# Kernel tuning notes

Measured on AMD Instinct MI355X. Metric: run time of the kernel, lower is better.

Reference implementation:

```python
import jax, jax.numpy as jnp
import numpy as np

N = 20000
E = 160000
H = 4      # heads
C = 128    # per-head out channels (hidden_dim)
HID = 128


def setup_inputs() -> dict:
    key = jax.random.key(0)
    ks = jax.random.split(key, 24)
    inp = {}
    inp["x"] = jax.random.normal(ks[0], (8,), jnp.float32)
    inp["des"] = jax.random.normal(ks[1], (N, 768), jnp.float32)
    inp["tweet"] = jax.random.normal(ks[2], (N, 768), jnp.float32)
    inp["num_prop"] = jax.random.normal(ks[3], (N, 5), jnp.float32)
    inp["cat_prop"] = jax.random.normal(ks[4], (N, 1), jnp.float32)
    inp["edge_index"] = jax.random.randint(ks[5], (2, E), 0, N, dtype=jnp.int64)
    inp["target_node_idx"] = 123
    s = lambda fan_in: 1.0 / np.sqrt(fan_in)
    u = lambda k, shp, b: jax.random.uniform(k, shp, jnp.float32, -b, b)
    inp["W_des"] = u(ks[6], (768, 32), s(768)); inp["b_des"] = u(ks[7], (32,), s(768))
    inp["W_tw"] = u(ks[8], (768, 32), s(768)); inp["b_tw"] = u(ks[9], (32,), s(768))
    inp["W_np"] = u(ks[10], (5, 32), s(5));   inp["b_np"] = u(ks[11], (32,), s(5))
    inp["W_cp"] = u(ks[12], (1, 32), s(1));   inp["b_cp"] = u(ks[13], (32,), s(1))
    inp["W_gat"] = u(ks[14], (HID, H * C), s(HID))      # GATConv lin (no bias)
    inp["att_src"] = u(ks[15], (H, C), s(C))
    inp["att_dst"] = u(ks[16], (H, C), s(C))
    inp["b_gat"] = jnp.zeros((C,), jnp.float32)
    inp["W_o1"] = u(ks[17], (HID + 8, 64), s(HID + 8)); inp["b_o1"] = u(ks[18], (64,), s(HID + 8))
    inp["W_o2"] = u(ks[19], (64, 5), s(64));            inp["b_o2"] = u(ks[20], (5,), s(64))
    return inp


def _gat_conv(feature, edge_index, W_gat, att_src, att_dst, b_gat):
    # add self-loops (PyG default)
    loops = jnp.arange(N, dtype=edge_index.dtype)
    src = jnp.concatenate([edge_index[0], loops])
    dst = jnp.concatenate([edge_index[1], loops])
    h = (feature @ W_gat).reshape(N, H, C)                 # [N,H,C]
    a_src = jnp.einsum("nhc,hc->nh", h, att_src)           # [N,H]
    a_dst = jnp.einsum("nhc,hc->nh", h, att_dst)
    e = jax.nn.leaky_relu(a_src[src] + a_dst[dst], 0.2)    # [E+N,H]
    m = jax.ops.segment_max(e, dst, num_segments=N)        # segment softmax (stable)
    ex = jnp.exp(e - m[dst])
    denom = jax.ops.segment_sum(ex, dst, num_segments=N)
    alpha = ex / denom[dst]                                # [E+N,H]
    out = jax.ops.segment_sum(alpha[:, :, None] * h[src], dst, num_segments=N)  # [N,H,C]
    return out.mean(axis=1) + b_gat                        # concat=False -> mean heads


def reference(x, des, tweet, num_prop, cat_prop, edge_index, target_node_idx,
              W_des, b_des, W_tw, b_tw, W_np, b_np, W_cp, b_cp,
              W_gat, att_src, att_dst, b_gat, W_o1, b_o1, W_o2, b_o2):
    lrelu = jax.nn.leaky_relu  # slope 0.01 (nn.LeakyReLU default)
    d = lrelu(des @ W_des + b_des)
    t = lrelu(tweet @ W_tw + b_tw)
    n = lrelu(num_prop @ W_np + b_np)
    c = lrelu(cat_prop @ W_cp + b_cp)
    feature = jnp.concatenate([d, t, n, c], axis=1)        # [N,128]
    gat_out = _gat_conv(feature, edge_index, W_gat, att_src, att_dst, b_gat)
    target_feat = gat_out[target_node_idx]                 # [128]
    combined = jnp.concatenate([target_feat, x], axis=0)   # [136]
    hmid = jax.nn.relu(combined @ W_o1 + b_o1)
    return hmid @ W_o2 + b_o2                              # [5]
```

## Files before the change

### kernel.cpp

```cpp
#include <hip/hip_runtime.h>
#include <math.h>

#define HEADS 4
#define CDIM 128
#define HDIM 512
#define FEAT 128
#define NBS 128
#define NT 512
#define REG 8
#define TGT_SID (NBS * REG)
#define NMAX 64

__global__ __launch_bounds__(NT)
void scan_process_kernel(const float* __restrict__ des, const float* __restrict__ tw,
                         const float* __restrict__ npr, const float* __restrict__ cpr,
                         const float* __restrict__ Wd, const float* __restrict__ bd,
                         const float* __restrict__ Wt, const float* __restrict__ bt,
                         const float* __restrict__ Wn, const float* __restrict__ bn,
                         const float* __restrict__ Wc, const float* __restrict__ bc,
                         const float* __restrict__ Wg, const float* __restrict__ Wo1,
                         const float* __restrict__ att_src, const float* __restrict__ att_dst,
                         const int* __restrict__ ei, int E,
                         const int* __restrict__ tgt_p,
                         int* __restrict__ blockCounts,
                         float* __restrict__ aS, float* __restrict__ aD,
                         float* __restrict__ h_all) {
    __shared__ float sdes[768];
    __shared__ float stw[768];
    __shared__ float snp8[8];
    __shared__ float sfeat[FEAT];
    __shared__ float part[NT];
    __shared__ float pr[2 * HDIM];
    __shared__ int   lmatch[REG];
    __shared__ int   lcount;

    const int tid = threadIdx.x;
    const int b = blockIdx.x;
    const int tgt = *tgt_p;
    const int wv = tid >> 6, lane = tid & 63;

    auto process_node = [&](int node, int sid, bool isTgt) {
        if (tid < 192) {
            ((float4*)sdes)[tid] = ((const float4*)(des + (size_t)node * 768))[tid];
            ((float4*)stw)[tid]  = ((const float4*)(tw  + (size_t)node * 768))[tid];
        } else if (tid < 197) {
            snp8[tid - 192] = npr[node * 5 + (tid - 192)];
        } else if (tid == 197) {
            snp8[5] = cpr[node];
        }
        __syncthreads();

        {
            const int half = tid >> 8;
            const int t2 = tid & 255;
            const int j = t2 & 31, ch = t2 >> 5;
            const float* W = half ? Wt : Wd;
            const float* S = half ? stw : sdes;
            const float* wp = W + (size_t)(ch * 96) * 32 + j;
            const float* sp = S + ch * 96;
            float p = 0.f;
            #pragma unroll 16
            for (int k = 0; k < 96; ++k) p = fmaf(sp[k], wp[(size_t)k * 32], p);
            part[tid] = p;
        }
        __syncthreads();
        if (tid < 32) {
            float a = bd[tid];
            #pragma unroll
            for (int c2 = 0; c2 < 8; ++c2) a += part[c2 * 32 + tid];
            sfeat[tid] = a > 0.f ? a : 0.01f * a;
        } else if (tid < 64) {
            const int jj = tid - 32;
            float a = bt[jj];
            #pragma unroll
            for (int c2 = 0; c2 < 8; ++c2) a += part[256 + c2 * 32 + jj];
            sfeat[32 + jj] = a > 0.f ? a : 0.01f * a;
        } else if (tid < 96) {
            const int jj = tid - 64;
            float a = bn[jj];
            #pragma unroll
            for (int k = 0; k < 5; ++k) a = fmaf(snp8[k], Wn[k * 32 + jj], a);
            sfeat[64 + jj] = a > 0.f ? a : 0.01f * a;
        } else if (tid < 128) {
            const int jj = tid - 96;
            float a = fmaf(snp8[5], Wc[jj], bc[jj]);
            sfeat[96 + jj] = a > 0.f ? a : 0.01f * a;
        }
        __syncthreads();

        {
            const float* wg = Wg + tid;
            float hv = 0.f;
            #pragma unroll 16
            for (int k = 0; k < FEAT; ++k) hv = fmaf(sfeat[k], wg[(size_t)k * HDIM], hv);
            h_all[(size_t)sid * HDIM + tid] = hv;
            pr[tid] = hv * att_src[tid];
            if (isTgt) pr[HDIM + tid] = hv * att_dst[tid];
        }
        __syncthreads();

        if (wv < 4) {
            float v = pr[wv * 128 + lane] + pr[wv * 128 + 64 + lane];
            #pragma unroll
            for (int off = 32; off > 0; off >>= 1) v += __shfl_down(v, off);
            if (lane == 0) aS[sid * HEADS + wv] = v;
        } else if (isTgt) {
            const int hd = wv - 4;
            float v = pr[HDIM + hd * 128 + lane] + pr[HDIM + hd * 128 + 64 + lane];
            #pragma unroll
            for (int off = 32; off > 0; off >>= 1) v += __shfl_down(v, off);
            if (lane == 0) aD[hd] = v;
        }
        __syncthreads();
    };

    if (b == NBS) {
        process_node(tgt, TGT_SID, true);
        return;
    }

    float keep = 0.f;
    {
        const int g = b * NT + tid;
        if (g < 6144)       { float4 v = ((const float4*)Wd)[g];           keep = v.x + v.y + v.z + v.w; }
        else if (g < 12288) { float4 v = ((const float4*)Wt)[g - 6144];    keep = v.x + v.y + v.z + v.w; }
        else if (g < 28672) { float4 v = ((const float4*)Wg)[g - 12288];   keep = v.x + v.y + v.z + v.w; }
        else if (g < 30848) { float4 v = ((const float4*)Wo1)[g - 28672];  keep = v.x + v.y + v.z + v.w; }
    }

    if (tid == 0) lcount = 0;
    __syncthreads();
    const int nquad = E >> 2;
    const int qb = (nquad + NBS - 1) / NBS;
    const int q0 = b * qb;
    const int qe = (q0 + qb < nquad) ? (q0 + qb) : nquad;
    for (int q = q0 + tid; q < qe; q += NT) {
        const int4 dd = *(const int4*)(ei + (size_t)E + (size_t)q * 4);
        const int base = q * 4;
        if (dd.x == tgt) { int p = atomicAdd(&lcount, 1); if (p < REG) lmatch[p] = ei[base + 0]; }
        if (dd.y == tgt) { int p = atomicAdd(&lcount, 1); if (p < REG) lmatch[p] = ei[base + 1]; }
        if (dd.z == tgt) { int p = atomicAdd(&lcount, 1); if (p < REG) lmatch[p] = ei[base + 2]; }
        if (dd.w == tgt) { int p = atomicAdd(&lcount, 1); if (p < REG) lmatch[p] = ei[base + 3]; }
    }
    if (b == NBS - 1) {
        for (int k = nquad * 4 + tid; k < E; k += NT)
            if (ei[E + k] == tgt) { int p = atomicAdd(&lcount, 1); if (p < REG) lmatch[p] = ei[k]; }
    }
    asm volatile("" :: "v"(keep));
    __syncthreads();

    const int mycount = (lcount < REG) ? lcount : REG;
    if (tid == 0) blockCounts[b] = mycount;

    for (int it = 0; it < mycount; ++it)
        process_node(lmatch[it], b * REG + it, false);
}

__global__ __launch_bounds__(NT)
void finalize_kernel(const float* __restrict__ x, const float* __restrict__ bgat,
                     const float* __restrict__ Wo1, const float* __restrict__ bo1,
                     const float* __restrict__ Wo2, const float* __restrict__ bo2,
                     const int* __restrict__ blockCounts,
                     const float* __restrict__ aS, const float* __restrict__ aD,
                     const float* __restrict__ h_all,
                     float* __restrict__ out) {
    __shared__ int   bc[NBS];
    __shared__ int   pf[NBS];
    __shared__ int   slots[NMAX];
    __shared__ float saS[NMAX * HEADS];
    __shared__ float saD[HEADS];
    __shared__ float pr[HDIM];
    __shared__ float scomb[144];
    __shared__ float shmid[64];
    __shared__ int   sM;

    const int tid = threadIdx.x;

    if (tid < NBS) { bc[tid] = blockCounts[tid]; pf[tid] = bc[tid]; }
    __syncthreads();
    for (int off = 1; off < NBS; off <<= 1) {
        int add = (tid < NBS && tid >= off) ? pf[tid - off] : 0;
        __syncthreads();
        if (tid < NBS) pf[tid] += add;
        __syncthreads();
    }
    if (tid < NBS) {
        const int excl = pf[tid] - bc[tid];
        for (int i = 0; i < bc[tid]; ++i) {
            const int p = excl + i;
            if (p < NMAX - 1) slots[p] = tid * REG + i;
        }
    }
    if (tid == 0) {
        int total = pf[NBS - 1];
        if (total > NMAX - 1) total = NMAX - 1;
        slots[total] = TGT_SID;
        sM = total + 1;
    }
    __syncthreads();
    const int M = sM;

    for (int i = tid; i < M * HEADS; i += NT) {
        const int s = i >> 2, hd = i & 3;
        saS[i] = aS[slots[s] * HEADS + hd];
    }
    if (tid < HEADS) saD[tid] = aD[tid];
    __syncthreads();

    {
        const int o = tid, hd = o >> 7;
        const float adv = saD[hd];
        float m = -INFINITY;
        for (int s = 0; s < M; ++s) {
            float e = saS[s * HEADS + hd] + adv;
            e = e > 0.f ? e : 0.2f * e;
            m = fmaxf(m, e);
        }
        float denom = 0.f, acc = 0.f;
        for (int s = 0; s < M; ++s) {
            float e = saS[s * HEADS + hd] + adv;
            e = e > 0.f ? e : 0.2f * e;
            const float ex = expf(e - m);
            denom += ex;
            acc = fmaf(ex, h_all[(size_t)slots[s] * HDIM + o], acc);
        }
        pr[o] = acc / denom;
    }
    __syncthreads();

    if (tid < 128) {
        scomb[tid] = (pr[tid] + pr[128 + tid] + pr[256 + tid] + pr[384 + tid]) * 0.25f
                     + bgat[tid];
    } else if (tid < 136) {
        scomb[tid] = x[tid - 128];
    }
    __syncthreads();

    if (tid < 64) {
        float a = bo1[tid];
        #pragma unroll 8
        for (int k = 0; k < 136; ++k) a = fmaf(scomb[k], Wo1[k * 64 + tid], a);
        shmid[tid] = a > 0.f ? a : 0.f;
    }
    __syncthreads();
    if (tid < 5) {
        float a = bo2[tid];
        #pragma unroll 8
        for (int k = 0; k < 64; ++k) a = fmaf(shmid[k], Wo2[k * 5 + tid], a);
        out[tid] = a;
    }
}

extern "C" void kernel_launch(void* const* d_in, const int* in_sizes, int n_in,
                              void* d_out, int out_size, void* d_ws, size_t ws_size,
                              hipStream_t stream) {
    const float* x    = (const float*)d_in[0];
    const float* des  = (const float*)d_in[1];
    const float* tw   = (const float*)d_in[2];
    const float* npr  = (const float*)d_in[3];
    const float* cpr  = (const float*)d_in[4];
    const int*   ei   = (const int*)d_in[5];
    const int*   tgt  = (const int*)d_in[6];
    const float* Wd   = (const float*)d_in[7];   const float* bd  = (const float*)d_in[8];
    const float* Wt   = (const float*)d_in[9];   const float* bt  = (const float*)d_in[10];
    const float* Wn   = (const float*)d_in[11];  const float* bn  = (const float*)d_in[12];
    const float* Wc   = (const float*)d_in[13];  const float* bc  = (const float*)d_in[14];
    const float* Wg   = (const float*)d_in[15];
    const float* as_  = (const float*)d_in[16];  const float* ad_ = (const float*)d_in[17];
    const float* bg   = (const float*)d_in[18];
    const float* Wo1  = (const float*)d_in[19];  const float* bo1 = (const float*)d_in[20];
    const float* Wo2  = (const float*)d_in[21];  const float* bo2 = (const float*)d_in[22];

    const int E = in_sizes[5] / 2;

    char* ws = (char*)d_ws;
    int*   blockCounts = (int*)ws;
    float* aS    = (float*)(ws + 1024);
    float* aD    = aS + (size_t)(TGT_SID + 1) * HEADS;
    float* h_all = aD + 16;

    scan_process_kernel<<<NBS + 1, NT, 0, stream>>>(des, tw, npr, cpr,
                                                    Wd, bd, Wt, bt, Wn, bn, Wc, bc,
                                                    Wg, Wo1, as_, ad_,
                                                    ei, E, tgt,
                                                    blockCounts, aS, aD, h_all);

    finalize_kernel<<<1, NT, 0, stream>>>(x, bg, Wo1, bo1, Wo2, bo2,
                                          blockCounts, aS, aD, h_all, (float*)d_out);
}
```

Baseline: 19.14 us.

## Double scan blocks, split FMA accumulators, and use wave-shuffle prefix scan

```diff
diff --git a/kernel.cpp b/kernel.cpp
--- a/kernel.cpp
+++ b/kernel.cpp
@@ -5,7 +5,7 @@
 #define CDIM 128
 #define HDIM 512
 #define FEAT 128
-#define NBS 128
+#define NBS 256
 #define NT 512
 #define REG 8
 #define TGT_SID (NBS * REG)
@@ -58,10 +58,13 @@
             const float* S = half ? stw : sdes;
             const float* wp = W + (size_t)(ch * 96) * 32 + j;
             const float* sp = S + ch * 96;
-            float p = 0.f;
-            #pragma unroll 16
-            for (int k = 0; k < 96; ++k) p = fmaf(sp[k], wp[(size_t)k * 32], p);
-            part[tid] = p;
+            float p0 = 0.f, p1 = 0.f;
+            #pragma unroll 24
+            for (int k = 0; k < 96; k += 2) {
+                p0 = fmaf(sp[k],     wp[(size_t)k * 32],       p0);
+                p1 = fmaf(sp[k + 1], wp[(size_t)(k + 1) * 32], p1);
+            }
+            part[tid] = p0 + p1;
         }
         __syncthreads();
         if (tid < 32) {
@@ -90,9 +93,13 @@
 
         {
             const float* wg = Wg + tid;
-            float hv = 0.f;
-            #pragma unroll 16
-            for (int k = 0; k < FEAT; ++k) hv = fmaf(sfeat[k], wg[(size_t)k * HDIM], hv);
+            float h0 = 0.f, h1 = 0.f;
+            #pragma unroll 32
+            for (int k = 0; k < FEAT; k += 2) {
+                h0 = fmaf(sfeat[k],     wg[(size_t)k * HDIM],       h0);
+                h1 = fmaf(sfeat[k + 1], wg[(size_t)(k + 1) * HDIM], h1);
+            }
+            const float hv = h0 + h1;
             h_all[(size_t)sid * HDIM + tid] = hv;
             pr[tid] = hv * att_src[tid];
             if (isTgt) pr[HDIM + tid] = hv * att_dst[tid];
@@ -164,8 +171,9 @@
                      const float* __restrict__ aS, const float* __restrict__ aD,
                      const float* __restrict__ h_all,
                      float* __restrict__ out) {
-    __shared__ int   bc[NBS];
+    __shared__ int   sbc[NBS];
     __shared__ int   pf[NBS];
+    __shared__ int   wtot[4];
     __shared__ int   slots[NMAX];
     __shared__ float saS[NMAX * HEADS];
     __shared__ float saD[HEADS];
@@ -175,18 +183,32 @@
     __shared__ int   sM;
 
     const int tid = threadIdx.x;
-
-    if (tid < NBS) { bc[tid] = blockCounts[tid]; pf[tid] = bc[tid]; }
-    __syncthreads();
-    for (int off = 1; off < NBS; off <<= 1) {
-        int add = (tid < NBS && tid >= off) ? pf[tid - off] : 0;
-        __syncthreads();
-        if (tid < NBS) pf[tid] += add;
-        __syncthreads();
-    }
+    const int lane = tid & 63;
+
     if (tid < NBS) {
-        const int excl = pf[tid] - bc[tid];
-        for (int i = 0; i < bc[tid]; ++i) {
+        const int v = blockCounts[tid];
+        sbc[tid] = v;
+        int s = v;
+        #pragma unroll
+        for (int off = 1; off < 64; off <<= 1) {
+            const int n = __shfl_up(s, off);
+            if (lane >= off) s += n;
+        }
+        pf[tid] = s;
+        if (lane == 63) wtot[tid >> 6] = s;
+    }
+    __syncthreads();
+    if (tid < NBS) {
+        const int w = tid >> 6;
+        int add = 0;
+        #pragma unroll
+        for (int p = 0; p < 3; ++p) if (w > p) add += wtot[p];
+        pf[tid] += add;
+    }
+    __syncthreads();
+    if (tid < NBS) {
+        const int excl = pf[tid] - sbc[tid];
+        for (int i = 0; i < sbc[tid]; ++i) {
             const int p = excl + i;
             if (p < NMAX - 1) slots[p] = tid * REG + i;
         }
@@ -275,7 +297,7 @@
 
     char* ws = (char*)d_ws;
     int*   blockCounts = (int*)ws;
-    float* aS    = (float*)(ws + 1024);
+    float* aS    = (float*)(ws + 2048);
     float* aD    = aS + (size_t)(TGT_SID + 1) * HEADS;
     float* h_all = aD + 16;
 
```

Measured after the change: 23.67 us. 1.24x slower.

## Prefetch matched neighbor rows during edge scan and use wave-shuffle prefix scan

Applied to the files above, without the earlier changes.

```diff
diff --git a/kernel.cpp b/kernel.cpp
--- a/kernel.cpp
+++ b/kernel.cpp
@@ -128,6 +128,13 @@
         else if (g < 30848) { float4 v = ((const float4*)Wo1)[g - 28672];  keep = v.x + v.y + v.z + v.w; }
     }
 
+    auto warm_rows = [&](int node) {
+        const float4* d4 = (const float4*)(des + (size_t)node * 768);
+        const float4* t4 = (const float4*)(tw  + (size_t)node * 768);
+        #pragma unroll
+        for (int t = 0; t < 192; t += 8) { keep += d4[t].x; keep += t4[t].x; }
+    };
+
     if (tid == 0) lcount = 0;
     __syncthreads();
     const int nquad = E >> 2;
@@ -137,14 +144,14 @@
     for (int q = q0 + tid; q < qe; q += NT) {
         const int4 dd = *(const int4*)(ei + (size_t)E + (size_t)q * 4);
         const int base = q * 4;
-        if (dd.x == tgt) { int p = atomicAdd(&lcount, 1); if (p < REG) lmatch[p] = ei[base + 0]; }
-        if (dd.y == tgt) { int p = atomicAdd(&lcount, 1); if (p < REG) lmatch[p] = ei[base + 1]; }
-        if (dd.z == tgt) { int p = atomicAdd(&lcount, 1); if (p < REG) lmatch[p] = ei[base + 2]; }
-        if (dd.w == tgt) { int p = atomicAdd(&lcount, 1); if (p < REG) lmatch[p] = ei[base + 3]; }
+        if (dd.x == tgt) { int p = atomicAdd(&lcount, 1); int n = ei[base + 0]; if (p < REG) lmatch[p] = n; warm_rows(n); }
+        if (dd.y == tgt) { int p = atomicAdd(&lcount, 1); int n = ei[base + 1]; if (p < REG) lmatch[p] = n; warm_rows(n); }
+        if (dd.z == tgt) { int p = atomicAdd(&lcount, 1); int n = ei[base + 2]; if (p < REG) lmatch[p] = n; warm_rows(n); }
+        if (dd.w == tgt) { int p = atomicAdd(&lcount, 1); int n = ei[base + 3]; if (p < REG) lmatch[p] = n; warm_rows(n); }
     }
     if (b == NBS - 1) {
         for (int k = nquad * 4 + tid; k < E; k += NT)
-            if (ei[E + k] == tgt) { int p = atomicAdd(&lcount, 1); if (p < REG) lmatch[p] = ei[k]; }
+            if (ei[E + k] == tgt) { int p = atomicAdd(&lcount, 1); int n = ei[k]; if (p < REG) lmatch[p] = n; warm_rows(n); }
     }
     asm volatile("" :: "v"(keep));
     __syncthreads();
@@ -164,7 +171,7 @@
                      const float* __restrict__ aS, const float* __restrict__ aD,
                      const float* __restrict__ h_all,
                      float* __restrict__ out) {
-    __shared__ int   bc[NBS];
+    __shared__ int   sbc[NBS];
     __shared__ int   pf[NBS];
     __shared__ int   slots[NMAX];
     __shared__ float saS[NMAX * HEADS];
@@ -176,17 +183,26 @@
 
     const int tid = threadIdx.x;
 
-    if (tid < NBS) { bc[tid] = blockCounts[tid]; pf[tid] = bc[tid]; }
-    __syncthreads();
-    for (int off = 1; off < NBS; off <<= 1) {
-        int add = (tid < NBS && tid >= off) ? pf[tid - off] : 0;
-        __syncthreads();
-        if (tid < NBS) pf[tid] += add;
-        __syncthreads();
-    }
+    if (tid < 64) {
+        const int v0 = blockCounts[2 * tid];
+        const int v1 = blockCounts[2 * tid + 1];
+        sbc[2 * tid] = v0;
+        sbc[2 * tid + 1] = v1;
+        int s = v0 + v1;
+        #pragma unroll
+        for (int off = 1; off < 64; off <<= 1) {
+            const int n = __shfl_up(s, off);
+            if (tid >= off) s += n;
+        }
+        pf[2 * tid]     = s - v1;
+        pf[2 * tid + 1] = s;
+    }
+    if (tid < HEADS) saD[tid] = aD[tid];
+    __syncthreads();
+
     if (tid < NBS) {
-        const int excl = pf[tid] - bc[tid];
-        for (int i = 0; i < bc[tid]; ++i) {
+        const int excl = pf[tid] - sbc[tid];
+        for (int i = 0; i < sbc[tid]; ++i) {
             const int p = excl + i;
             if (p < NMAX - 1) slots[p] = tid * REG + i;
         }
@@ -204,7 +220,6 @@
         const int s = i >> 2, hd = i & 3;
         saS[i] = aS[slots[s] * HEADS + hd];
     }
-    if (tid < HEADS) saD[tid] = aD[tid];
     __syncthreads();
 
     {
```

Result: no change. 19.45 us (+1.7%).
